# Optimization experiments

Hardware: AMD Instinct MI355X
Metric: run time of the kernel (lower is better)

## Reference

```python
import jax, jax.numpy as jnp
import numpy as np

B, A, N, P = 1024, 25, 250, 250  # batch, NUM_AGENTS, graph_size, num patrol nodes


def setup_inputs() -> dict:
    key = jax.random.key(0)
    k1, k2, k3, k4 = jax.random.split(key, 4)
    state = jax.random.normal(k1, (B, A, N, 3), dtype=jnp.float32)
    nodes_coords = jax.random.normal(k2, (P, 2), dtype=jnp.float32)
    adj = jax.random.uniform(k3, (P, N), dtype=jnp.float32)
    node_last_visit = jax.random.randint(k4, (B, A), 0, P, dtype=jnp.int32)
    patrol_index = jnp.arange(P, dtype=jnp.int32)  # obsMap.patrol_nodes.index lookup table
    return {
        'state': state,
        'nodes_coords': nodes_coords,
        'adj': adj,
        'node_last_visit': node_last_visit,
        'patrol_index': patrol_index,
    }


def reference(state, nodes_coords, adj, node_last_visit, patrol_index):
    # Vectorized form of the nested per-(batch, agent) Python loops in Policy.forward:
    #   zuobiao[i, j] = obsMap.nodes[node_last_visit[i, j]]
    #   idx[i, j]     = patrol_nodes.index(node_last_visit[i, j])
    #   mask[i, j]    = adj[idx[i, j]]
    zuobiao = nodes_coords[node_last_visit]          # [B, A, 2]
    idx = patrol_index[node_last_visit]              # [B, A]
    mask = adj[idx]                                  # [B, A, N]
    # zuobiao broadcast over graph_size, then concat onto state (pads features 3 -> 5)
    zb = jnp.broadcast_to(zuobiao[:, :, None, :], (B, A, N, 2))
    state_cat = jnp.concatenate([state, zb], axis=-1)            # [B, A, N, 5]
    # Pack mask as an extra channel so the fused gather pipeline has one output.
    out = jnp.concatenate([state_cat, mask[..., None]], axis=-1)  # [B, A, N, 6]
    return out
```

## Files before the change

kernel.cpp:

```cpp
#include <hip/hip_runtime.h>

#define BB 1024
#define AA 25
#define NN 250
#define PP 250
#define BA (BB * AA)
#define GROUPS 125
#define BLOCKS 1600
#define TPB 256

typedef float v2f __attribute__((ext_vector_type(2)));
typedef float v4f __attribute__((ext_vector_type(4)));

__global__ __launch_bounds__(TPB) void policy_kernel(
    const float* __restrict__ state,
    const float* __restrict__ nodes_coords,
    const float* __restrict__ adj,
    const int*   __restrict__ nlv,
    const int*   __restrict__ patrol_index,
    float* __restrict__ out)
{
    const int tid    = threadIdx.x;
    const int lane   = tid & 63;
    const int wave   = (blockIdx.x << 2) | (tid >> 6);
    const int nwaves = BLOCKS << 2;

    for (int ba = wave; ba < BA; ba += nwaves) {
        const int nv  = __builtin_amdgcn_readfirstlane(nlv[ba]);
        const int idx = __builtin_amdgcn_readfirstlane(patrol_index[nv]);
        const float zx = nodes_coords[2 * nv + 0];
        const float zy = nodes_coords[2 * nv + 1];

        const v2f* st2 = (const v2f*)(state + (size_t)ba * (NN * 3));
        const v2f* ad2 = (const v2f*)(adj + (size_t)idx * NN);
        v4f* op4 = (v4f*)(out + (size_t)ba * (NN * 6));

        for (int g = lane; g < GROUPS; g += 64) {
            v2f s0 = __builtin_nontemporal_load(&st2[3 * g + 0]);
            v2f s1 = __builtin_nontemporal_load(&st2[3 * g + 1]);
            v2f s2 = __builtin_nontemporal_load(&st2[3 * g + 2]);
            v2f a  = ad2[g];

            v4f v0 = {s0.x, s0.y, s1.x, zx};
            v4f v1 = {zy, a.x, s1.y, s2.x};
            v4f v2 = {s2.y, zx, zy, a.y};

            __builtin_nontemporal_store(v0, &op4[3 * g + 0]);
            __builtin_nontemporal_store(v1, &op4[3 * g + 1]);
            __builtin_nontemporal_store(v2, &op4[3 * g + 2]);
        }
    }
}

extern "C" void kernel_launch(void* const* d_in, const int* in_sizes, int n_in,
                              void* d_out, int out_size, void* d_ws, size_t ws_size,
                              hipStream_t stream) {
    const float* state        = (const float*)d_in[0];
    const float* nodes_coords = (const float*)d_in[1];
    const float* adj          = (const float*)d_in[2];
    const int*   nlv          = (const int*)d_in[3];
    const int*   patrol_index = (const int*)d_in[4];
    float* out = (float*)d_out;

    policy_kernel<<<dim3(BLOCKS), dim3(TPB), 0, stream>>>(
        state, nodes_coords, adj, nlv, patrol_index, out);
}
```

Before: 243.3 us.

## Stage two rows per block in LDS for fully coalesced 16-byte loads and stores

Each block now handles two (batch, agent) rows. It first copies their state into shared memory with 16-byte vector loads and gathers the adjacency rows into LDS, then each thread writes one consecutive 16-byte output vector, so stores are fully contiguous across lanes. This replaces the earlier one-wave-per-row grid-stride loop, which used strided 8-byte loads and three strided 16-byte stores per lane. The cost is an extra LDS round trip, a __syncthreads per block, a much larger grid of 12800 blocks, and the loss of the nontemporal load and store hints.

```diff
diff --git a/kernel.cpp b/kernel.cpp
--- a/kernel.cpp
+++ b/kernel.cpp
@@ -5,8 +5,6 @@
 #define NN 250
 #define PP 250
 #define BA (BB * AA)
-#define GROUPS 125
-#define BLOCKS 1600
 #define TPB 256
 
 typedef float v2f __attribute__((ext_vector_type(2)));
@@ -20,35 +18,57 @@
     const int*   __restrict__ patrol_index,
     float* __restrict__ out)
 {
-    const int tid    = threadIdx.x;
-    const int lane   = tid & 63;
-    const int wave   = (blockIdx.x << 2) | (tid >> 6);
-    const int nwaves = BLOCKS << 2;
+    __shared__ float s_state[2 * NN * 3];
+    __shared__ float s_adj[2 * NN];
+    __shared__ float s_z[4];
 
-    for (int ba = wave; ba < BA; ba += nwaves) {
-        const int nv  = __builtin_amdgcn_readfirstlane(nlv[ba]);
-        const int idx = __builtin_amdgcn_readfirstlane(patrol_index[nv]);
-        const float zx = nodes_coords[2 * nv + 0];
-        const float zy = nodes_coords[2 * nv + 1];
+    const int tid = threadIdx.x;
+    const int ba0 = blockIdx.x * 2;
 
-        const v2f* st2 = (const v2f*)(state + (size_t)ba * (NN * 3));
+    {
+        const v4f* st4 = (const v4f*)(state + (size_t)ba0 * (NN * 3));
+        v4f* ss4 = (v4f*)s_state;
+        for (int i = tid; i < (2 * NN * 3) / 4; i += TPB)
+            ss4[i] = st4[i];
+    }
+
+    {
+        const int r = tid >> 7;
+        const int j = tid & 127;
+        const int ba = ba0 + r;
+        const int nv  = nlv[ba];
+        const int idx = patrol_index[nv];
+        if (j == 0) {
+            s_z[2 * r + 0] = nodes_coords[2 * nv + 0];
+            s_z[2 * r + 1] = nodes_coords[2 * nv + 1];
+        }
         const v2f* ad2 = (const v2f*)(adj + (size_t)idx * NN);
-        v4f* op4 = (v4f*)(out + (size_t)ba * (NN * 6));
+        if (j < NN / 2)
+            ((v2f*)(s_adj + r * NN))[j] = ad2[j];
+    }
+    __syncthreads();
 
-        for (int g = lane; g < GROUPS; g += 64) {
-            v2f s0 = __builtin_nontemporal_load(&st2[3 * g + 0]);
-            v2f s1 = __builtin_nontemporal_load(&st2[3 * g + 1]);
-            v2f s2 = __builtin_nontemporal_load(&st2[3 * g + 2]);
-            v2f a  = ad2[g];
+    const float zx0 = s_z[0], zy0 = s_z[1], zx1 = s_z[2], zy1 = s_z[3];
 
-            v4f v0 = {s0.x, s0.y, s1.x, zx};
-            v4f v1 = {zy, a.x, s1.y, s2.x};
-            v4f v2 = {s2.y, zx, zy, a.y};
-
-            __builtin_nontemporal_store(v0, &op4[3 * g + 0]);
-            __builtin_nontemporal_store(v1, &op4[3 * g + 1]);
-            __builtin_nontemporal_store(v2, &op4[3 * g + 2]);
+    v4f* op4 = (v4f*)(out + (size_t)ba0 * (NN * 6));
+    for (int q = tid; q < 2 * (NN * 6) / 4; q += TPB) {
+        const int row = (q >= 375);
+        const int ql  = q - 375 * row;
+        const int g   = ql / 3;
+        const int r   = ql - 3 * g;
+        const float* sp = s_state + row * (NN * 3) + 6 * g;
+        const float* ap = s_adj + row * NN + 2 * g;
+        const float zx = row ? zx1 : zx0;
+        const float zy = row ? zy1 : zy0;
+        v4f v;
+        if (r == 0) {
+            v = (v4f){sp[0], sp[1], sp[2], zx};
+        } else if (r == 1) {
+            v = (v4f){zy, ap[0], sp[3], sp[4]};
+        } else {
+            v = (v4f){sp[5], zx, zy, ap[1]};
         }
+        op4[q] = v;
     }
 }
 
@@ -62,6 +82,6 @@
     const int*   patrol_index = (const int*)d_in[4];
     float* out = (float*)d_out;
 
-    policy_kernel<<<dim3(BLOCKS), dim3(TPB), 0, stream>>>(
+    policy_kernel<<<dim3(BA / 2), dim3(TPB), 0, stream>>>(
         state, nodes_coords, adj, nlv, patrol_index, out);
 }
```

Measured after the change: 223.6 us. -8.1%, faster.
